# Optimization experiments

Hardware: AMD Instinct MI355X
Metric: run time of the kernel (lower is better)

Reference implementation:

```python
import jax, jax.numpy as jnp
import numpy as np

N_CLASSES = 10
N_INTERNAL = 256
ELEMS_PER_NODE = 3


def build_circuit(seed=0):
    """Deterministic SDD-like DAG in topological order.
    Node ids: 0..9 = positive class literals, 10..19 = negated literals,
    20.. = internal decision nodes. Each decision node is a list of
    (prime_id, sub_id) element pairs; primes are distinct positive literals
    (mutually-exclusive events) so node values stay bounded in [0,1]."""
    rng = np.random.RandomState(seed)
    n_base = 2 * N_CLASSES
    nodes = []
    for i in range(N_INTERNAL):
        avail = n_base + i
        primes = rng.choice(N_CLASSES, size=ELEMS_PER_NODE, replace=False)
        subs = rng.randint(0, avail, size=ELEMS_PER_NODE)
        nodes.append([(int(p), int(s)) for p, s in zip(primes, subs)])
    return nodes

CIRCUIT = build_circuit(0)


def eval_sdd(probs):
    # probs: [B, 10] softmax outputs. WMC semiring: (add, mul, 0, 1).
    vals = [probs[:, v] for v in range(N_CLASSES)]
    vals += [1.0 - probs[:, v] for v in range(N_CLASSES)]
    for elems in CIRCUIT:
        acc = vals[elems[0][0]] * vals[elems[0][1]]
        for p, s in elems[1:]:
            acc = acc + vals[p] * vals[s]
        vals.append(acc)
    return vals[-1]  # root node, shape [B]


def setup_inputs() -> dict:
    key = jax.random.key(0)
    ks = jax.random.split(key, 7)
    B, D_IN, H, C = 8192, 784, 4096, N_CLASSES
    s1 = 1.0 / np.sqrt(D_IN)
    s2 = 1.0 / np.sqrt(H)
    return {
        "x": jax.random.normal(ks[0], (B, D_IN), dtype=jnp.float32),
        "W1": jax.random.uniform(ks[1], (D_IN, H), jnp.float32, -s1, s1),
        "b1": jnp.zeros((H,), jnp.float32),
        "W2": jax.random.uniform(ks[2], (H, H), jnp.float32, -s2, s2),
        "b2": jnp.zeros((H,), jnp.float32),
        "W3": jax.random.uniform(ks[3], (H, C), jnp.float32, -s2, s2),
        "b3": jnp.zeros((C,), jnp.float32),
    }


def reference(x, W1, b1, W2, b2, W3, b3):
    h = jax.nn.relu(x @ W1 + b1)          # [B, H]
    h = jax.nn.relu(h @ W2 + b2)          # [B, H]
    logits = h @ W3 + b3                  # [B, 10]
    probs = jax.nn.softmax(logits, axis=-1)
    return eval_sdd(probs)                # [B]
```

## Files before the change

kernel.cpp:

```cpp
#include <hip/hip_runtime.h>
#include <cstdint>
#include <cstddef>

constexpr int N_CLASSES  = 10;
constexpr int N_INTERNAL = 256;
constexpr int N_VALS     = 2 * N_CLASSES + N_INTERNAL;
constexpr int B_SZ  = 8192;
constexpr int D_IN  = 784;
constexpr int KP1   = 896;
constexpr int H_DIM = 4096;

struct MTState {
  uint32_t key[624];
  int pos;
};

constexpr uint32_t mt_next(MTState& st) {
  if (st.pos == 624) {
    for (int i = 0; i < 624; ++i) {
      uint32_t y = (st.key[i] & 0x80000000u) | (st.key[(i + 1) % 624] & 0x7fffffffu);
      st.key[i] = st.key[(i + 397) % 624] ^ (y >> 1) ^ ((y & 1u) ? 0x9908b0dfu : 0u);
    }
    st.pos = 0;
  }
  uint32_t y = st.key[st.pos++];
  y ^= y >> 11;
  y ^= (y << 7) & 0x9d2c5680u;
  y ^= (y << 15) & 0xefc60000u;
  y ^= y >> 18;
  return y;
}

constexpr uint32_t interval_draw(MTState& st, uint32_t maxv) {
  if (maxv == 0u) return 0u;
  uint32_t mask = maxv;
  mask |= mask >> 1; mask |= mask >> 2; mask |= mask >> 4;
  mask |= mask >> 8; mask |= mask >> 16;
  uint32_t v = mt_next(st) & mask;
  while (v > maxv) v = mt_next(st) & mask;
  return v;
}

struct Circuit {
  int16_t prime[N_INTERNAL][3];
  int16_t sub[N_INTERNAL][3];
};

constexpr Circuit make_circuit() {
  MTState st{};
  uint32_t s = 0u;
  for (int i = 0; i < 624; ++i) {
    st.key[i] = s;
    s = 1812433253u * (s ^ (s >> 30)) + (uint32_t)i + 1u;
  }
  st.pos = 624;

  Circuit c{};
  for (int node = 0; node < N_INTERNAL; ++node) {
    const int avail = 2 * N_CLASSES + node;
    int arr[N_CLASSES] = {0, 1, 2, 3, 4, 5, 6, 7, 8, 9};
    for (int i = N_CLASSES - 1; i >= 1; --i) {
      uint32_t j = interval_draw(st, (uint32_t)i);
      int tmp = arr[i]; arr[i] = arr[j]; arr[j] = tmp;
    }
    for (int e = 0; e < 3; ++e) c.prime[node][e] = (int16_t)arr[e];
    for (int e = 0; e < 3; ++e) c.sub[node][e] = (int16_t)interval_draw(st, (uint32_t)(avail - 1));
  }
  return c;
}

constexpr Circuit CIRC = make_circuit();

__device__ __forceinline__ uint16_t f2bf(float f) {
  uint32_t u = __builtin_bit_cast(uint32_t, f);
  uint32_t r = (u + 0x7fffu + ((u >> 16) & 1u)) >> 16;
  return (uint16_t)r;
}
__device__ __forceinline__ float bf2f(uint16_t h) {
  uint32_t u = ((uint32_t)h) << 16;
  return __builtin_bit_cast(float, u);
}

__device__ __forceinline__ void load_lds16(const void* g, void* l) {
  __builtin_amdgcn_global_load_lds(
      (const __attribute__((address_space(1))) unsigned int*)g,
      (__attribute__((address_space(3))) unsigned int*)l, 16, 0, 0);
}

using bf16x8 = __attribute__((ext_vector_type(8))) short;
using f32x4  = __attribute__((ext_vector_type(4))) float;
using u16x8  = __attribute__((ext_vector_type(8))) unsigned short;
using u16x4  = __attribute__((ext_vector_type(4))) unsigned short;

template <int IMM>
__device__ __forceinline__ void dsr_i(bf16x8& d, uint32_t a) {
  asm volatile("ds_read_b128 %0, %1 offset:%2" : "=v"(d) : "v"(a), "n"(IMM));
}

template <int I>
__device__ __forceinline__ void eval_node(float (&vals)[N_VALS]) {
  if constexpr (I < N_INTERNAL) {
    constexpr int p0 = CIRC.prime[I][0], s0 = CIRC.sub[I][0];
    constexpr int p1 = CIRC.prime[I][1], s1 = CIRC.sub[I][1];
    constexpr int p2 = CIRC.prime[I][2], s2 = CIRC.sub[I][2];
    vals[2 * N_CLASSES + I] =
        vals[p0] * vals[s0] + vals[p1] * vals[s1] + vals[p2] * vals[s2];
    eval_node<I + 1>(vals);
  }
}

__global__ __launch_bounds__(256) void circuit_kernel(
    const float* __restrict__ probs, float* __restrict__ out, int B) {
  int r = blockIdx.x * blockDim.x + threadIdx.x;
  if (r >= B) return;
  float vals[N_VALS];
#pragma unroll
  for (int c = 0; c < N_CLASSES; ++c) {
    float p = probs[r * N_CLASSES + c];
    vals[c] = p;
    vals[N_CLASSES + c] = 1.0f - p;
  }
  eval_node<0>(vals);
  out[r] = vals[N_VALS - 1];
}

__global__ __launch_bounds__(256) void convert_pad_x(
    const float* __restrict__ x, uint16_t* __restrict__ xb) {
  const int r = blockIdx.x;
  const int t = threadIdx.x;
  if (t < D_IN / 4) {
    float4 v = *reinterpret_cast<const float4*>(x + (size_t)r * D_IN + t * 4);
    u16x4 o;
    o[0] = f2bf(v.x); o[1] = f2bf(v.y); o[2] = f2bf(v.z); o[3] = f2bf(v.w);
    *reinterpret_cast<u16x4*>(xb + (size_t)r * KP1 + t * 4) = o;
  } else if (t < KP1 / 4) {
    u16x4 z = {0, 0, 0, 0};
    *reinterpret_cast<u16x4*>(xb + (size_t)r * KP1 + t * 4) = z;
  }
}

__global__ __launch_bounds__(256) void transpose_convert(
    const float* __restrict__ W, uint16_t* __restrict__ Wt,
    int K, int N, int Kp) {
  __shared__ float tile[64][65];
  const int kt = blockIdx.y * 64;
  const int nt = blockIdx.x * 64;
  const int t  = threadIdx.x;

  const int lr = t >> 4;
  const int lc = (t & 15) * 4;
#pragma unroll
  for (int p = 0; p < 4; ++p) {
    const int row = lr + p * 16;
    const int k = kt + row;
    float4 v = {0.f, 0.f, 0.f, 0.f};
    if (k < K) v = *reinterpret_cast<const float4*>(W + (size_t)k * N + nt + lc);
    tile[row][lc + 0] = v.x;
    tile[row][lc + 1] = v.y;
    tile[row][lc + 2] = v.z;
    tile[row][lc + 3] = v.w;
  }
  __syncthreads();

  const int wn = t >> 3;
  const int k8 = (t & 7) * 8;
#pragma unroll
  for (int p = 0; p < 2; ++p) {
    const int n = nt + wn + 32 * p;
    u16x8 o;
#pragma unroll
    for (int i = 0; i < 8; ++i) o[i] = f2bf(tile[k8 + i][wn + 32 * p]);
    *reinterpret_cast<u16x8*>(Wt + (size_t)n * Kp + kt + k8) = o;
  }
}

template <int MH, int NH, int BUF, bool RA, bool RB, int VM, typename F>
__device__ __forceinline__ void phase_t(
    uint32_t aA0, uint32_t aA1, uint32_t bA0, uint32_t bA1,
    bf16x8 (&Ar)[4][2], bf16x8 (&Br)[2][2][2], f32x4 (&acc)[2][2][4][2],
    F&& stage) {
  constexpr int AO = BUF * 32768 + MH * 16384;
  constexpr int BO = BUF * 32768 + NH * 16384;
  if constexpr (RA) {
    dsr_i<AO + 0 * 2048>(Ar[0][0], aA0); dsr_i<AO + 0 * 2048>(Ar[0][1], aA1);
    dsr_i<AO + 1 * 2048>(Ar[1][0], aA0); dsr_i<AO + 1 * 2048>(Ar[1][1], aA1);
    dsr_i<AO + 2 * 2048>(Ar[2][0], aA0); dsr_i<AO + 2 * 2048>(Ar[2][1], aA1);
    dsr_i<AO + 3 * 2048>(Ar[3][0], aA0); dsr_i<AO + 3 * 2048>(Ar[3][1], aA1);
  }
  if constexpr (RB) {
    dsr_i<BO + 0 * 2048>(Br[NH][0][0], bA0); dsr_i<BO + 0 * 2048>(Br[NH][0][1], bA1);
    dsr_i<BO + 1 * 2048>(Br[NH][1][0], bA0); dsr_i<BO + 1 * 2048>(Br[NH][1][1], bA1);
  }
  stage();
  asm volatile("s_waitcnt lgkmcnt(0)" ::: "memory");
  __builtin_amdgcn_sched_barrier(0);
  __builtin_amdgcn_s_setprio(1);
#pragma unroll
  for (int m = 0; m < 4; ++m)
#pragma unroll
    for (int nf = 0; nf < 2; ++nf) {
      acc[MH][NH][m][nf] = __builtin_amdgcn_mfma_f32_16x16x32_bf16(
          Ar[m][0], Br[NH][nf][0], acc[MH][NH][m][nf], 0, 0, 0);
      acc[MH][NH][m][nf] = __builtin_amdgcn_mfma_f32_16x16x32_bf16(
          Ar[m][1], Br[NH][nf][1], acc[MH][NH][m][nf], 0, 0, 0);
    }
  __builtin_amdgcn_s_setprio(0);
  if constexpr (VM >= 0) asm volatile("s_waitcnt vmcnt(%0)" :: "i"(VM) : "memory");
  __builtin_amdgcn_s_barrier();
}

__global__ __launch_bounds__(512, 1) void gemm256_bf16(
    const uint16_t* __restrict__ A, const uint16_t* __restrict__ Bt,
    const float* __restrict__ bias, uint16_t* __restrict__ C,
    int M, int N, int K) {
  extern __shared__ char smem[];

  const int t    = threadIdx.x;
  const int t16  = t * 16;
  const int lane = t & 63;
  const int wid  = t >> 6;
  const int wr   = wid >> 2;
  const int wc   = wid & 3;
  const int fr   = lane & 15;
  const int fq   = lane >> 4;

  const int gx = gridDim.x, gy = gridDim.y;
  const int nwg = gx * gy;
  const int id  = blockIdx.y * gx + blockIdx.x;
  const int cpx = nwg >> 3;
  const int sid = (id & 7) * cpx + (id >> 3);
  const int row0 = (sid / gx) * 256;
  const int col0 = (sid % gx) * 256;

  const uint32_t Kb = (uint32_t)K * 2;

  const char* gA = (const char*)A + (size_t)row0 * Kb;
  const char* gB = (const char*)Bt + (size_t)col0 * Kb;

  const uint32_t prow = (uint32_t)(t >> 3);
  const uint32_t sg   = (uint32_t)(((t & 7) ^ (t >> 3)) & 7) * 16u;
  const uint32_t srcA = prow * Kb + sg;
  const uint32_t srcB = (prow + 32u * (prow >> 5)) * Kb + sg;

#define ROWA(h, j) ((h) * 64 + (j) * 128)
#define ROWB(h, j) ((h) * 32 + (j) * 128)

#define STAGE_A(v, h, kt) do { \
    load_lds16(gA + (size_t)(kt) * 128 + (size_t)ROWA(h, 0) * Kb + srcA, \
               smem + (v) * 32768 + (h) * 16384 + t16); \
    load_lds16(gA + (size_t)(kt) * 128 + (size_t)ROWA(h, 1) * Kb + srcA, \
               smem + (v) * 32768 + (h) * 16384 + 8192 + t16); } while (0)
#define STAGE_B(v, h, kt) do { \
    load_lds16(gB + (size_t)(kt) * 128 + (size_t)ROWB(h, 0) * Kb + srcB, \
               smem + 65536 + (v) * 32768 + (h) * 16384 + t16); \
    load_lds16(gB + (size_t)(kt) * 128 + (size_t)ROWB(h, 1) * Kb + srcB, \
               smem + 65536 + (v) * 32768 + (h) * 16384 + 8192 + t16); } while (0)

  const uint32_t smb = (uint32_t)(size_t)(__attribute__((address_space(3))) char*)smem;
  const uint32_t s0v = (uint32_t)(((fq) ^ (fr & 7)) * 16);
  const uint32_t aA0 = smb + (uint32_t)((wr * 64 + fr) * 128) + s0v;
  const uint32_t aA1 = smb + (uint32_t)((wr * 64 + fr) * 128) + (s0v ^ 64u);
  const uint32_t bA0 = smb + 65536u + (uint32_t)((wc * 32 + fr) * 128) + s0v;
  const uint32_t bA1 = smb + 65536u + (uint32_t)((wc * 32 + fr) * 128) + (s0v ^ 64u);

  f32x4 acc[2][2][4][2];
#pragma unroll
  for (int a = 0; a < 2; ++a)
#pragma unroll
    for (int b = 0; b < 2; ++b)
#pragma unroll
      for (int m = 0; m < 4; ++m)
#pragma unroll
        for (int n = 0; n < 2; ++n) {
          acc[a][b][m][n][0] = 0.f; acc[a][b][m][n][1] = 0.f;
          acc[a][b][m][n][2] = 0.f; acc[a][b][m][n][3] = 0.f;
        }

  bf16x8 Ar[4][2], Br[2][2][2];

  STAGE_A(0, 0, 0); STAGE_B(0, 0, 0); STAGE_A(0, 1, 0); STAGE_B(0, 1, 0);
  STAGE_A(1, 0, 1); STAGE_B(1, 1, 1); STAGE_A(1, 1, 1);
  asm volatile("s_waitcnt vmcnt(6)" ::: "memory");
  __builtin_amdgcn_s_barrier();

#define PH(MH_, NH_, RA_, RB_, VM_, BUF_, ...) \
  phase_t<MH_, NH_, BUF_, RA_, RB_, VM_>(aA0, aA1, bA0, bA1, \
                                         Ar, Br, acc, [&]() { __VA_ARGS__ })

  const int NI = K >> 7;
  int i = 0;
  for (; i < NI - 1; ++i) {
    const int ktb = 2 * i + 1, ktc = 2 * i + 2, ktd = 2 * i + 3;
    PH(0, 0, true,  true,  -1, 0, STAGE_B(1, 0, ktb); );
    PH(0, 1, false, true,  -1, 0, STAGE_A(0, 0, ktc); );
    PH(1, 1, true,  false, -1, 0, STAGE_B(0, 1, ktc); );
    PH(1, 0, false, true,   6, 0, STAGE_A(0, 1, ktc); );
    PH(0, 0, true,  true,  -1, 1, STAGE_B(0, 0, ktc); );
    PH(0, 1, false, true,  -1, 1, STAGE_A(1, 0, ktd); );
    PH(1, 1, true,  false, -1, 1, STAGE_B(1, 1, ktd); );
    PH(1, 0, false, true,   6, 1, STAGE_A(1, 1, ktd); );
  }
  {
    const int ktb = 2 * i + 1;
    PH(0, 0, true,  true,  -1, 0, STAGE_B(1, 0, ktb); );
    PH(0, 1, false, true,  -1, 0, );
    PH(1, 1, true,  false, -1, 0, );
    PH(1, 0, false, true,   0, 0, );
    PH(0, 0, true,  true,  -1, 1, );
    PH(0, 1, false, true,  -1, 1, );
    PH(1, 1, true,  false, -1, 1, );
    PH(1, 0, false, true,  -1, 1, );
  }
#undef PH
#undef STAGE_A
#undef STAGE_B
#undef ROWA
#undef ROWB

#pragma unroll
  for (int mh = 0; mh < 2; ++mh)
#pragma unroll
    for (int nh = 0; nh < 2; ++nh)
#pragma unroll
      for (int m = 0; m < 4; ++m)
#pragma unroll
        for (int nf = 0; nf < 2; ++nf) {
          const int row = row0 + wr * 128 + mh * 64 + m * 16 + fq * 4;
          const int col = col0 + wc * 64 + nh * 32 + nf * 16 + fr;
          const float bv = bias[col];
          const size_t base = (size_t)row * N + col;
#pragma unroll
          for (int j = 0; j < 4; ++j) {
            float v = acc[mh][nh][m][nf][j] + bv;
            v = fmaxf(v, 0.0f);
            C[base + (size_t)j * N] = f2bf(v);
          }
        }
}

__global__ __launch_bounds__(256) void logits_softmax_kernel(
    const uint16_t* __restrict__ h2, const float* __restrict__ W3,
    const float* __restrict__ b3, float* __restrict__ probs, int B) {
  const int wave = threadIdx.x >> 6;
  const int lane = threadIdx.x & 63;
  const int row  = blockIdx.x * 4 + wave;
  if (row >= B) return;

  const uint16_t* hrow = h2 + (size_t)row * H_DIM;
  float acc[N_CLASSES];
#pragma unroll
  for (int c = 0; c < N_CLASSES; ++c) acc[c] = 0.0f;

#pragma unroll
  for (int it = 0; it < H_DIM / (64 * 8); ++it) {
    const int k0 = (it * 64 + lane) * 8;
    ushort4 u0 = *reinterpret_cast<const ushort4*>(hrow + k0);
    ushort4 u1 = *reinterpret_cast<const ushort4*>(hrow + k0 + 4);
    float hv[8] = {bf2f(u0.x), bf2f(u0.y), bf2f(u0.z), bf2f(u0.w),
                   bf2f(u1.x), bf2f(u1.y), bf2f(u1.z), bf2f(u1.w)};
#pragma unroll
    for (int q = 0; q < 8; ++q) {
      const float* wrow = W3 + (size_t)(k0 + q) * N_CLASSES;
#pragma unroll
      for (int c = 0; c < N_CLASSES; ++c) acc[c] = fmaf(hv[q], wrow[c], acc[c]);
    }
  }

#pragma unroll
  for (int c = 0; c < N_CLASSES; ++c) {
#pragma unroll
    for (int s = 32; s >= 1; s >>= 1) acc[c] += __shfl_xor(acc[c], s, 64);
  }

  if (lane == 0) {
    float l[N_CLASSES], m = -3.0e38f;
#pragma unroll
    for (int c = 0; c < N_CLASSES; ++c) {
      l[c] = acc[c] + b3[c];
      m = fmaxf(m, l[c]);
    }
    float sum = 0.0f;
#pragma unroll
    for (int c = 0; c < N_CLASSES; ++c) {
      l[c] = expf(l[c] - m);
      sum += l[c];
    }
    const float inv = 1.0f / sum;
#pragma unroll
    for (int c = 0; c < N_CLASSES; ++c) probs[row * N_CLASSES + c] = l[c] * inv;
  }
}

extern "C" void kernel_launch(void* const* d_in, const int* in_sizes, int n_in,
                              void* d_out, int out_size, void* d_ws, size_t ws_size,
                              hipStream_t stream) {
  const float* x  = (const float*)d_in[0];
  const float* W1 = (const float*)d_in[1];
  const float* b1 = (const float*)d_in[2];
  const float* W2 = (const float*)d_in[3];
  const float* b2 = (const float*)d_in[4];
  const float* W3 = (const float*)d_in[5];
  const float* b3 = (const float*)d_in[6];
  float* out = (float*)d_out;

  uint16_t* xb  = (uint16_t*)d_ws;
  uint16_t* w1t = xb  + (size_t)B_SZ * KP1;
  uint16_t* w2t = w1t + (size_t)H_DIM * KP1;
  uint16_t* h1  = w2t + (size_t)H_DIM * H_DIM;
  uint16_t* h2  = h1  + (size_t)B_SZ * H_DIM;
  float* probs  = (float*)(h2 + (size_t)B_SZ * H_DIM);

  (void)hipFuncSetAttribute((const void*)gemm256_bf16,
                            hipFuncAttributeMaxDynamicSharedMemorySize, 131072);

  dim3 blk(256);

  convert_pad_x<<<dim3(B_SZ), blk, 0, stream>>>(x, xb);
  transpose_convert<<<dim3(H_DIM / 64, KP1 / 64), blk, 0, stream>>>(W1, w1t, D_IN, H_DIM, KP1);
  transpose_convert<<<dim3(H_DIM / 64, H_DIM / 64), blk, 0, stream>>>(W2, w2t, H_DIM, H_DIM, H_DIM);

  gemm256_bf16<<<dim3(H_DIM / 256, B_SZ / 256), dim3(512), 131072, stream>>>(
      xb, w1t, b1, h1, B_SZ, H_DIM, KP1);

  gemm256_bf16<<<dim3(H_DIM / 256, B_SZ / 256), dim3(512), 131072, stream>>>(
      h1, w2t, b2, h2, B_SZ, H_DIM, H_DIM);

  logits_softmax_kernel<<<dim3(B_SZ / 4), blk, 0, stream>>>(h2, W3, b3, probs, B_SZ);

  circuit_kernel<<<dim3(B_SZ / 256), blk, 0, stream>>>(probs, out, B_SZ);
}
```

Measured before the change: 402.6 us.

## Switch GEMM to 32x32x16 MFMA with simplified two-stage k-tile pipeline

Replaces the 16x16x32 bf16 MFMA tiling with 32x32x16 MFMAs that accumulate into 16-float fragments, which means fewer LDS fragment reads per FLOP. The fine-grained eight-phase schedule, which interleaved half-tile loads, is replaced by four phases per iteration that load whole k-tiles into alternating buffers and wait on vmcnt(0). The intent is higher MFMA efficiency and lower LDS traffic. The cost is less overlap between global loads and compute, plus a more scattered epilogue store pattern.

```diff
diff --git a/kernel.cpp b/kernel.cpp
--- a/kernel.cpp
+++ b/kernel.cpp
@@ -89,6 +89,7 @@
 
 using bf16x8 = __attribute__((ext_vector_type(8))) short;
 using f32x4  = __attribute__((ext_vector_type(4))) float;
+using f32x16 = __attribute__((ext_vector_type(16))) float;
 using u16x8  = __attribute__((ext_vector_type(8))) unsigned short;
 using u16x4  = __attribute__((ext_vector_type(4))) unsigned short;
 
@@ -174,38 +175,35 @@
   }
 }
 
-template <int MH, int NH, int BUF, bool RA, bool RB, int VM, typename F>
-__device__ __forceinline__ void phase_t(
-    uint32_t aA0, uint32_t aA1, uint32_t bA0, uint32_t bA1,
-    bf16x8 (&Ar)[4][2], bf16x8 (&Br)[2][2][2], f32x4 (&acc)[2][2][4][2],
-    F&& stage) {
-  constexpr int AO = BUF * 32768 + MH * 16384;
-  constexpr int BO = BUF * 32768 + NH * 16384;
-  if constexpr (RA) {
-    dsr_i<AO + 0 * 2048>(Ar[0][0], aA0); dsr_i<AO + 0 * 2048>(Ar[0][1], aA1);
-    dsr_i<AO + 1 * 2048>(Ar[1][0], aA0); dsr_i<AO + 1 * 2048>(Ar[1][1], aA1);
-    dsr_i<AO + 2 * 2048>(Ar[2][0], aA0); dsr_i<AO + 2 * 2048>(Ar[2][1], aA1);
-    dsr_i<AO + 3 * 2048>(Ar[3][0], aA0); dsr_i<AO + 3 * 2048>(Ar[3][1], aA1);
-  }
-  if constexpr (RB) {
-    dsr_i<BO + 0 * 2048>(Br[NH][0][0], bA0); dsr_i<BO + 0 * 2048>(Br[NH][0][1], bA1);
-    dsr_i<BO + 1 * 2048>(Br[NH][1][0], bA0); dsr_i<BO + 1 * 2048>(Br[NH][1][1], bA1);
-  }
+__device__ __forceinline__ f32x16 mfma32(const bf16x8& a, const bf16x8& b, const f32x16& c) {
+  return __builtin_amdgcn_mfma_f32_32x32x16_bf16(a, b, c, 0, 0, 0);
+}
+
+template <int BUF, int SP, typename F>
+__device__ __forceinline__ void phase32(
+    const uint32_t (&aA)[4], const uint32_t (&bA)[4],
+    f32x16 (&acc)[4][2], F&& stage) {
+  constexpr int BO = BUF * 32768;
+  bf16x8 Af[4][2], Bf[2][2];
+  dsr_i<BO + 0>(Af[0][0], aA[SP]);     dsr_i<BO + 0>(Af[0][1], aA[SP + 1]);
+  dsr_i<BO + 4096>(Af[1][0], aA[SP]);  dsr_i<BO + 4096>(Af[1][1], aA[SP + 1]);
+  dsr_i<BO + 16384>(Af[2][0], aA[SP]); dsr_i<BO + 16384>(Af[2][1], aA[SP + 1]);
+  dsr_i<BO + 20480>(Af[3][0], aA[SP]); dsr_i<BO + 20480>(Af[3][1], aA[SP + 1]);
+  dsr_i<BO + 0>(Bf[0][0], bA[SP]);     dsr_i<BO + 0>(Bf[0][1], bA[SP + 1]);
+  dsr_i<BO + 16384>(Bf[1][0], bA[SP]); dsr_i<BO + 16384>(Bf[1][1], bA[SP + 1]);
   stage();
   asm volatile("s_waitcnt lgkmcnt(0)" ::: "memory");
   __builtin_amdgcn_sched_barrier(0);
   __builtin_amdgcn_s_setprio(1);
 #pragma unroll
-  for (int m = 0; m < 4; ++m)
-#pragma unroll
-    for (int nf = 0; nf < 2; ++nf) {
-      acc[MH][NH][m][nf] = __builtin_amdgcn_mfma_f32_16x16x32_bf16(
-          Ar[m][0], Br[NH][nf][0], acc[MH][NH][m][nf], 0, 0, 0);
-      acc[MH][NH][m][nf] = __builtin_amdgcn_mfma_f32_16x16x32_bf16(
-          Ar[m][1], Br[NH][nf][1], acc[MH][NH][m][nf], 0, 0, 0);
-    }
+  for (int sl = 0; sl < 2; ++sl)
+#pragma unroll
+    for (int rt = 0; rt < 4; ++rt)
+#pragma unroll
+      for (int ct = 0; ct < 2; ++ct)
+        acc[rt][ct] = mfma32(Af[rt][sl], Bf[ct][sl], acc[rt][ct]);
   __builtin_amdgcn_s_setprio(0);
-  if constexpr (VM >= 0) asm volatile("s_waitcnt vmcnt(%0)" :: "i"(VM) : "memory");
+  if constexpr (SP == 2) asm volatile("s_waitcnt vmcnt(0)" ::: "memory");
   __builtin_amdgcn_s_barrier();
 }
 
@@ -221,8 +219,9 @@
   const int wid  = t >> 6;
   const int wr   = wid >> 2;
   const int wc   = wid & 3;
-  const int fr   = lane & 15;
-  const int fq   = lane >> 4;
+  const int l31  = lane & 31;
+  const int hi   = lane >> 5;
+  const int l7   = lane & 7;
 
   const int gx = gridDim.x, gy = gridDim.y;
   const int nwg = gx * gy;
@@ -257,85 +256,71 @@
                smem + 65536 + (v) * 32768 + (h) * 16384 + 8192 + t16); } while (0)
 
   const uint32_t smb = (uint32_t)(size_t)(__attribute__((address_space(3))) char*)smem;
-  const uint32_t s0v = (uint32_t)(((fq) ^ (fr & 7)) * 16);
-  const uint32_t aA0 = smb + (uint32_t)((wr * 64 + fr) * 128) + s0v;
-  const uint32_t aA1 = smb + (uint32_t)((wr * 64 + fr) * 128) + (s0v ^ 64u);
-  const uint32_t bA0 = smb + 65536u + (uint32_t)((wc * 32 + fr) * 128) + s0v;
-  const uint32_t bA1 = smb + 65536u + (uint32_t)((wc * 32 + fr) * 128) + (s0v ^ 64u);
-
-  f32x4 acc[2][2][4][2];
-#pragma unroll
-  for (int a = 0; a < 2; ++a)
-#pragma unroll
-    for (int b = 0; b < 2; ++b)
-#pragma unroll
-      for (int m = 0; m < 4; ++m)
-#pragma unroll
-        for (int n = 0; n < 2; ++n) {
-          acc[a][b][m][n][0] = 0.f; acc[a][b][m][n][1] = 0.f;
-          acc[a][b][m][n][2] = 0.f; acc[a][b][m][n][3] = 0.f;
-        }
-
-  bf16x8 Ar[4][2], Br[2][2][2];
+  uint32_t aA[4], bA[4];
+  const uint32_t abase = smb + (uint32_t)(wr * 8192 + l31 * 128);
+  const uint32_t bbase = smb + 65536u +
+      (uint32_t)((wc >> 1) * 8192 + (wc & 1) * 4096 + l31 * 128);
+#pragma unroll
+  for (int s = 0; s < 4; ++s) {
+    const uint32_t slot = (uint32_t)(((s * 2) | hi) ^ l7) * 16u;
+    aA[s] = abase + slot;
+    bA[s] = bbase + slot;
+  }
+
+  f32x16 acc[4][2];
+#pragma unroll
+  for (int rt = 0; rt < 4; ++rt)
+#pragma unroll
+    for (int ct = 0; ct < 2; ++ct)
+#pragma unroll
+      for (int e = 0; e < 16; ++e) acc[rt][ct][e] = 0.0f;
 
   STAGE_A(0, 0, 0); STAGE_B(0, 0, 0); STAGE_A(0, 1, 0); STAGE_B(0, 1, 0);
-  STAGE_A(1, 0, 1); STAGE_B(1, 1, 1); STAGE_A(1, 1, 1);
-  asm volatile("s_waitcnt vmcnt(6)" ::: "memory");
+  asm volatile("s_waitcnt vmcnt(0)" ::: "memory");
   __builtin_amdgcn_s_barrier();
-
-#define PH(MH_, NH_, RA_, RB_, VM_, BUF_, ...) \
-  phase_t<MH_, NH_, BUF_, RA_, RB_, VM_>(aA0, aA1, bA0, bA1, \
-                                         Ar, Br, acc, [&]() { __VA_ARGS__ })
 
   const int NI = K >> 7;
   int i = 0;
   for (; i < NI - 1; ++i) {
-    const int ktb = 2 * i + 1, ktc = 2 * i + 2, ktd = 2 * i + 3;
-    PH(0, 0, true,  true,  -1, 0, STAGE_B(1, 0, ktb); );
-    PH(0, 1, false, true,  -1, 0, STAGE_A(0, 0, ktc); );
-    PH(1, 1, true,  false, -1, 0, STAGE_B(0, 1, ktc); );
-    PH(1, 0, false, true,   6, 0, STAGE_A(0, 1, ktc); );
-    PH(0, 0, true,  true,  -1, 1, STAGE_B(0, 0, ktc); );
-    PH(0, 1, false, true,  -1, 1, STAGE_A(1, 0, ktd); );
-    PH(1, 1, true,  false, -1, 1, STAGE_B(1, 1, ktd); );
-    PH(1, 0, false, true,   6, 1, STAGE_A(1, 1, ktd); );
+    const int tb = 2 * i + 1, tc = 2 * i + 2;
+    phase32<0, 0>(aA, bA, acc, [&]() {
+      STAGE_A(1, 0, tb); STAGE_B(1, 0, tb); STAGE_A(1, 1, tb); STAGE_B(1, 1, tb);
+    });
+    phase32<0, 2>(aA, bA, acc, [&]() {});
+    phase32<1, 0>(aA, bA, acc, [&]() {
+      STAGE_A(0, 0, tc); STAGE_B(0, 0, tc); STAGE_A(0, 1, tc); STAGE_B(0, 1, tc);
+    });
+    phase32<1, 2>(aA, bA, acc, [&]() {});
   }
   {
-    const int ktb = 2 * i + 1;
-    PH(0, 0, true,  true,  -1, 0, STAGE_B(1, 0, ktb); );
-    PH(0, 1, false, true,  -1, 0, );
-    PH(1, 1, true,  false, -1, 0, );
-    PH(1, 0, false, true,   0, 0, );
-    PH(0, 0, true,  true,  -1, 1, );
-    PH(0, 1, false, true,  -1, 1, );
-    PH(1, 1, true,  false, -1, 1, );
-    PH(1, 0, false, true,  -1, 1, );
-  }
-#undef PH
+    const int tb = 2 * i + 1;
+    phase32<0, 0>(aA, bA, acc, [&]() {
+      STAGE_A(1, 0, tb); STAGE_B(1, 0, tb); STAGE_A(1, 1, tb); STAGE_B(1, 1, tb);
+    });
+    phase32<0, 2>(aA, bA, acc, [&]() {});
+    phase32<1, 0>(aA, bA, acc, [&]() {});
+    phase32<1, 2>(aA, bA, acc, [&]() {});
+  }
 #undef STAGE_A
 #undef STAGE_B
 #undef ROWA
 #undef ROWB
 
 #pragma unroll
-  for (int mh = 0; mh < 2; ++mh)
-#pragma unroll
-    for (int nh = 0; nh < 2; ++nh)
-#pragma unroll
-      for (int m = 0; m < 4; ++m)
-#pragma unroll
-        for (int nf = 0; nf < 2; ++nf) {
-          const int row = row0 + wr * 128 + mh * 64 + m * 16 + fq * 4;
-          const int col = col0 + wc * 64 + nh * 32 + nf * 16 + fr;
-          const float bv = bias[col];
-          const size_t base = (size_t)row * N + col;
-#pragma unroll
-          for (int j = 0; j < 4; ++j) {
-            float v = acc[mh][nh][m][nf][j] + bv;
-            v = fmaxf(v, 0.0f);
-            C[base + (size_t)j * N] = f2bf(v);
-          }
-        }
+  for (int rt = 0; rt < 4; ++rt)
+#pragma unroll
+    for (int ct = 0; ct < 2; ++ct) {
+      const int col = col0 + wc * 64 + ct * 32 + l31;
+      const float bv = bias[col];
+#pragma unroll
+      for (int reg = 0; reg < 16; ++reg) {
+        const int row = row0 + wr * 128 + rt * 32 +
+                        (reg & 3) + 8 * (reg >> 2) + 4 * hi;
+        float v = acc[rt][ct][reg] + bv;
+        v = fmaxf(v, 0.0f);
+        C[(size_t)row * N + col] = f2bf(v);
+      }
+    }
 }
 
 __global__ __launch_bounds__(256) void logits_softmax_kernel(
```

Measured after the change: 448.5 us. +11.4%, slower.
